# Kernel tuning notes

Hardware: AMD Instinct MI355X
Metric: run time of the kernel (lower is better)

The kernel has to match this reference:

```python
import jax, jax.numpy as jnp
import numpy as np

N_QUBITS = 6
N_SHARED_LAYERS = 3
N_TASK_LAYERS = 2
ENC_HIDDEN = 256
INPUT_DIM = 784
BATCH = 256
P1Q = 0.001  # 1-qubit depolarizing prob
P2Q = 0.01   # 2-qubit-gate depolarizing approximation (applied as 1q channel, as in source)

C = jnp.complex64
PX = jnp.array([[0, 1], [1, 0]], C)
PY = jnp.array([[0, -1j], [1j, 0]], C)
PZ = jnp.array([[1, 0], [0, -1]], C)
CNOT = jnp.array([[1, 0, 0, 0], [0, 1, 0, 0], [0, 0, 0, 1], [0, 0, 1, 0]], C)

_LOW = 'abcdefghijklmnopqrstuvwxyz'


def _apply(dm, G, axes, batched):
    # contract gate G (rows=out, cols=in) into dm along absolute dm axes `axes`
    k = len(axes)
    G = G.reshape(G.shape[:G.ndim - 2] + (2,) * (2 * k))
    nd = dm.ndim - 1  # 2 * n_qubits
    dm_sub = ['Z'] + list(_LOW[:nd])
    out_sub = list(dm_sub)
    new = 'ABCD'
    gout, gin = [], []
    for j, ax in enumerate(axes):
        gout.append(new[j]); gin.append(dm_sub[ax]); out_sub[ax] = new[j]
    g_str = ('Z' if batched else '') + ''.join(gout) + ''.join(gin)
    return jnp.einsum(f"{g_str},{''.join(dm_sub)}->{''.join(out_sub)}", G, dm)


def apply_unitary(dm, U, wires, n, batched=False):
    # rho -> U rho U^dagger; ket axes are 1+w, bra axes 1+n+w
    dm = _apply(dm, U, [1 + w for w in wires], batched)
    return _apply(dm, jnp.conj(U), [1 + n + w for w in wires], batched)


def depolarize(dm, p, q, n):
    x = apply_unitary(dm, PX, [q], n)
    y = apply_unitary(dm, PY, [q], n)
    z = apply_unitary(dm, PZ, [q], n)
    return (1.0 - p) * dm + (p / 3.0) * (x + y + z)


def rot_mat(phi, theta, omega):
    # PennyLane Rot(phi, theta, omega) = RZ(omega) RY(theta) RZ(phi)
    c = jnp.cos(theta / 2)
    s = jnp.sin(theta / 2)
    ep = jnp.exp(-0.5j * (phi + omega))  # e^{-i(phi+omega)/2}
    em = jnp.exp(0.5j * (phi - omega))   # e^{+i(phi-omega)/2}
    return jnp.stack([jnp.stack([ep * c, -em * s]),
                      jnp.stack([jnp.conj(em) * s, jnp.conj(ep) * c])]).astype(C)


def ry_batched(theta):
    # theta: (B,) -> (B,2,2)
    c = jnp.cos(theta / 2)
    s = jnp.sin(theta / 2)
    return jnp.stack([jnp.stack([c, -s], -1),
                      jnp.stack([s, c], -1)], -2).astype(C)


def strongly_entangling(dm, w, n):
    # PennyLane StronglyEntanglingLayers, default ranges r = (l % (n-1)) + 1, CNOT ring
    L = w.shape[0]
    for l in range(L):
        for i in range(n):
            dm = apply_unitary(dm, rot_mat(w[l, i, 0], w[l, i, 1], w[l, i, 2]), [i], n)
        r = (l % (n - 1)) + 1
        for i in range(n):
            dm = apply_unitary(dm, CNOT, [i, (i + r) % n], n)
    return dm


def circuit(z, shared_w, task_w):
    n = N_QUBITS
    Bz = z.shape[0]
    dm = jnp.zeros((Bz,) + (2,) * (2 * n), C).at[(slice(None),) + (0,) * (2 * n)].set(1.0)
    for i in range(n):
        dm = apply_unitary(dm, ry_batched(z[:, i] * jnp.pi), [i], n, batched=True)
        dm = depolarize(dm, P1Q, i, n)
    dm = strongly_entangling(dm, shared_w, n)
    for i in range(n):
        dm = depolarize(dm, P1Q, i, n)
    for i in range(n - 1):
        dm = depolarize(dm, P2Q, i, n)
    dm = strongly_entangling(dm, task_w, n)
    for i in range(n):
        dm = depolarize(dm, P1Q, i, n)
    D = 2 ** n
    probs = jnp.real(jnp.diagonal(dm.reshape(Bz, D, D), axis1=1, axis2=2))  # (B, D)
    bits = (jnp.arange(D)[:, None] >> jnp.arange(n - 1, -1, -1)[None, :]) & 1  # wire 0 = MSB
    signs = (1 - 2 * bits).astype(jnp.float32)  # (D, n)
    return probs.astype(jnp.float32) @ signs    # (B, n) = <Z_i>


def setup_inputs():
    key = jax.random.key(0)
    ks = jax.random.split(key, 8)
    f = jnp.float32
    return {
        "x": jax.random.normal(ks[0], (BATCH, INPUT_DIM), f),
        "W1": jax.random.normal(ks[1], (ENC_HIDDEN, INPUT_DIM), f) * 0.03,
        "b1": jnp.zeros((ENC_HIDDEN,), f),
        "ln_g": jnp.ones((ENC_HIDDEN,), f),
        "ln_b": jnp.zeros((ENC_HIDDEN,), f),
        "W2": jax.random.normal(ks[2], (N_QUBITS, ENC_HIDDEN), f) * 0.05,
        "b2": jnp.zeros((N_QUBITS,), f),
        "shared_w": jax.random.normal(ks[3], (N_SHARED_LAYERS, N_QUBITS, 3), f) * 0.1,
        "task_w": jax.random.normal(ks[4], (N_TASK_LAYERS, N_QUBITS, 3), f) * 0.1,
        "Wp": jax.random.normal(ks[5], (2, N_QUBITS), f) * 0.1,
        "bp": jnp.zeros((2,), f),
    }


def reference(x, W1, b1, ln_g, ln_b, W2, b2, shared_w, task_w, Wp, bp):
    # encoder: Linear -> ReLU -> LayerNorm -> Linear -> Tanh
    h = jnp.maximum(x @ W1.T + b1, 0.0)
    mu = h.mean(-1, keepdims=True)
    var = ((h - mu) ** 2).mean(-1, keepdims=True)
    h = (h - mu) / jnp.sqrt(var + 1e-5) * ln_g + ln_b
    z = jnp.tanh(h @ W2.T + b2)            # (B, N_QUBITS)
    ev = circuit(z, shared_w, task_w)      # (B, N_QUBITS)
    return ev @ Wp.T + bp                  # (B, 2)
```

## Files before the change

### kernel.cpp

```cpp
#include <hip/hip_runtime.h>
#include <math.h>

#define NQ 6
#define BLK 1024
#define HID 256
#define INDIM 784

#define PW1 0.001f
#define PW2 0.01f
constexpr float WO1 = 1.f - 4.f * PW1 / 3.f;
constexpr float WO2 = 1.f - 4.f * PW2 / 3.f;
constexpr float WOc = WO1 * WO2;

struct alignas(16) RingTabs { int t[3][4096]; };
constexpr RingTabs make_ring_tabs() {
    RingTabs R{};
    for (int ri = 0; ri < 3; ++ri) {
        int r = ri + 1;
        for (int v = 0; v < 4096; ++v) {
            int x[6], z[6];
            for (int w = 0; w < 6; ++w) { x[w] = (v >> (2 * w + 1)) & 1; z[w] = (v >> (2 * w)) & 1; }
            int sgn = 0;
            for (int i = 5; i >= 0; --i) {
                int c = i, tg = (i + r) % 6;
                sgn ^= x[c] & z[tg] & (x[tg] ^ z[c] ^ 1);
                x[tg] ^= x[c];
                z[c]  ^= z[tg];
            }
            int s = 0;
            for (int w = 0; w < 6; ++w) s |= (x[w] << (2 * w + 1)) | (z[w] << (2 * w));
            R.t[ri][v] = s | (sgn << 31);
        }
    }
    return R;
}
static __device__ const RingTabs RT = make_ring_tabs();

__device__ __forceinline__ int swz(int n) {
    return n ^ ((((n >> 6) ^ (n >> 10)) & 3) << 3);
}

template<int CTRL>
__device__ __forceinline__ float qb(float v) {
    int r = __builtin_amdgcn_update_dpp(0, __builtin_bit_cast(int, v), CTRL, 0xF, 0xF, true);
    return __builtin_bit_cast(float, r);
}

__device__ __forceinline__ void rot_reg(float e[4], float4 rZ, float4 rX, float4 rY) {
    float X = e[2], Y = e[3], Z = e[1];
    e[2] = fmaf(rX.x, X, fmaf(rX.y, Y, rX.z * Z));
    e[3] = fmaf(rY.x, X, fmaf(rY.y, Y, rY.z * Z));
    e[1] = fmaf(rZ.x, X, fmaf(rZ.y, Y, rZ.z * Z));
}

__device__ __forceinline__ void rot_lane(float e[4], float4 cf) {
    #pragma unroll
    for (int j = 0; j < 4; ++j) {
        float vZ = qb<0x55>(e[j]);
        float vX = qb<0xAA>(e[j]);
        float vY = qb<0xFF>(e[j]);
        e[j] = fmaf(cf.x, vX, fmaf(cf.y, vY, fmaf(cf.z, vZ, cf.w * e[j])));
    }
}


__global__ __launch_bounds__(BLK)
void nqm_kernel(const float* __restrict__ x, const float* __restrict__ W1,
                const float* __restrict__ b1, const float* __restrict__ ln_g,
                const float* __restrict__ ln_b, const float* __restrict__ W2,
                const float* __restrict__ b2, const float* __restrict__ shared_w,
                const float* __restrict__ task_w, const float* __restrict__ Wp,
                const float* __restrict__ bp, float* __restrict__ out)
{
    __shared__ __align__(16) float dm[4096];
    __shared__ float4 xrow[INDIM / 4];
    __shared__ float hpart[1024];
    __shared__ __align__(16) float4 Mlane[30][4];
    __shared__ float bloch[NQ][4];
    __shared__ float red[4], red2[4];
    __shared__ float zpart[4][8];
    __shared__ float bcast[2];
    __shared__ float evs[8];

    const int tid = threadIdx.x;
    const int b = blockIdx.x;
    const int lane = tid & 63;
    const int qpos = tid & 3;

    if (tid < INDIM / 4) xrow[tid] = ((const float4*)(x + (size_t)b * INDIM))[tid];
    __syncthreads();

    {
        const int u = tid & 255, p = tid >> 8;
        const float4* w1v = (const float4*)(W1 + (size_t)u * INDIM) + p * 49;
        const float4* xv4 = xrow + p * 49;
        float acc = 0.0f;
        #pragma unroll 7
        for (int k = 0; k < 49; ++k) {
            float4 wv = w1v[k];
            float4 xv = xv4[k];
            acc = fmaf(wv.x, xv.x, acc);
            acc = fmaf(wv.y, xv.y, acc);
            acc = fmaf(wv.z, xv.z, acc);
            acc = fmaf(wv.w, xv.w, acc);
        }
        hpart[p * 256 + u] = acc;
    }
    __syncthreads();

    float h = 0.0f;
    if (tid < 256) {
        h = hpart[tid] + hpart[256 + tid] + hpart[512 + tid] + hpart[768 + tid] + b1[tid];
        h = fmaxf(h, 0.0f);
        float s = h, s2 = h * h;
        #pragma unroll
        for (int off = 32; off > 0; off >>= 1) {
            s  += __shfl_down(s, off, 64);
            s2 += __shfl_down(s2, off, 64);
        }
        if (lane == 0) { red[tid >> 6] = s; red2[tid >> 6] = s2; }
    }
    __syncthreads();
    if (tid == 0) {
        float ts  = red[0] + red[1] + red[2] + red[3];
        float ts2 = red2[0] + red2[1] + red2[2] + red2[3];
        float mu  = ts * (1.0f / HID);
        float var = ts2 * (1.0f / HID) - mu * mu;
        bcast[0] = mu;
        bcast[1] = rsqrtf(var + 1e-5f);
    }
    __syncthreads();
    if (tid < 256) {
        float hnj = (h - bcast[0]) * bcast[1] * ln_g[tid] + ln_b[tid];
        float p[NQ];
        #pragma unroll
        for (int i = 0; i < NQ; ++i) p[i] = hnj * W2[i * HID + tid];
        #pragma unroll
        for (int off = 32; off > 0; off >>= 1) {
            #pragma unroll
            for (int i = 0; i < NQ; ++i) p[i] += __shfl_down(p[i], off, 64);
        }
        if (lane == 0) {
            #pragma unroll
            for (int i = 0; i < NQ; ++i) zpart[tid >> 6][i] = p[i];
        }
    }
    __syncthreads();

    if (tid < NQ) {
        float z = zpart[0][tid] + zpart[1][tid] + zpart[2][tid] + zpart[3][tid] + b2[tid];
        z = tanhf(z);
        float sn, c;
        sincosf(z * 3.14159265358979323846f, &sn, &c);
        bloch[tid][0] = 1.0f;
        bloch[tid][1] = WO1 * c;
        bloch[tid][2] = WO1 * sn;
        bloch[tid][3] = 0.0f;
    } else if (tid < 36) {
        int g = tid - NQ;
        int layer = g / NQ;
        int wire = g % NQ;
        const float* w = (layer < 3) ? (shared_w + (layer * NQ + wire) * 3)
                                     : (task_w + ((layer - 3) * NQ + wire) * 3);
        float phi = w[0], theta = w[1], omega = w[2];
        float sf, cf_, st, ct, so, co;
        sincosf(phi, &sf, &cf_);
        sincosf(theta, &st, &ct);
        sincosf(omega, &so, &co);
        float M00 = co * ct * cf_ - so * sf;
        float M01 = -co * ct * sf - so * cf_;
        float M02 = co * st;
        float M10 = so * ct * cf_ + co * sf;
        float M11 = -so * ct * sf + co * cf_;
        float M12 = so * st;
        float M20 = -st * cf_;
        float M21 = st * sf;
        float M22 = ct;
        float f = (layer == 3) ? ((wire < 5) ? WOc : WO1) : 1.0f;
        Mlane[g][0] = make_float4(0.f, 0.f, 0.f, 1.f);
        Mlane[g][1] = make_float4(f * M20, f * M21, f * M22, 0.f);
        Mlane[g][2] = make_float4(f * M00, f * M01, f * M02, 0.f);
        Mlane[g][3] = make_float4(f * M10, f * M11, f * M12, 0.f);
    }

    const int t = tid;
    const int base1 = ((t & 0x3C0) << 2) | ((t & 3) << 6) | ((t >> 2) & 0xF);
    const int base2 = ((t & 3) << 10) | ((t >> 2) & 0xFF);
    __syncthreads();

    const int rtab[4] = {0, 1, 2, 0};
    for (int l = 0; l < 5; ++l) {
        const int g0 = l * 6;
        float e[4];

        if (l == 0) {
            float A = bloch[1][t & 3] * bloch[2][(t >> 2) & 3] * bloch[3][(t >> 4) & 3]
                    * bloch[4][(t >> 6) & 3] * bloch[5][(t >> 8) & 3];
            e[0] = A * bloch[0][0];
            e[1] = A * bloch[0][1];
            e[2] = A * bloch[0][2];
            e[3] = A * bloch[0][3];
        } else {
            const int4 te = *(const int4*)&RT.t[rtab[l - 1]][t << 2];
            float v0 = dm[swz(te.x & 4095)];
            float v1 = dm[swz(te.y & 4095)];
            float v2 = dm[swz(te.z & 4095)];
            float v3 = dm[swz(te.w & 4095)];
            e[0] = __int_as_float(__float_as_int(v0) ^ (te.x & 0x80000000));
            e[1] = __int_as_float(__float_as_int(v1) ^ (te.y & 0x80000000));
            e[2] = __int_as_float(__float_as_int(v2) ^ (te.z & 0x80000000));
            e[3] = __int_as_float(__float_as_int(v3) ^ (te.w & 0x80000000));
            __syncthreads();
        }
        {
            float4 rZ = Mlane[g0 + 0][1], rX = Mlane[g0 + 0][2], rY = Mlane[g0 + 0][3];
            rot_reg(e, rZ, rX, rY);
            rot_lane(e, Mlane[g0 + 1][qpos]);
        }
        *(float4*)&dm[swz(t << 2)] = make_float4(e[0], e[1], e[2], e[3]);
        __syncthreads();

        e[0] = dm[swz(base1)];
        e[1] = dm[swz(base1 + 16)];
        e[2] = dm[swz(base1 + 32)];
        e[3] = dm[swz(base1 + 48)];
        {
            float4 rZ = Mlane[g0 + 2][1], rX = Mlane[g0 + 2][2], rY = Mlane[g0 + 2][3];
            rot_reg(e, rZ, rX, rY);
            rot_lane(e, Mlane[g0 + 3][qpos]);
        }
        dm[swz(base1)]      = e[0];
        dm[swz(base1 + 16)] = e[1];
        dm[swz(base1 + 32)] = e[2];
        dm[swz(base1 + 48)] = e[3];
        __syncthreads();

        e[0] = dm[swz(base2)];
        e[1] = dm[swz(base2 + 256)];
        e[2] = dm[swz(base2 + 512)];
        e[3] = dm[swz(base2 + 768)];
        {
            float4 rZ = Mlane[g0 + 4][1], rX = Mlane[g0 + 4][2], rY = Mlane[g0 + 4][3];
            rot_reg(e, rZ, rX, rY);
            rot_lane(e, Mlane[g0 + 5][qpos]);
        }
        dm[swz(base2)]       = e[0];
        dm[swz(base2 + 256)] = e[1];
        dm[swz(base2 + 512)] = e[2];
        dm[swz(base2 + 768)] = e[3];
        __syncthreads();
    }

    if (tid < NQ) {
        int e = RT.t[1][1 << (2 * tid)];
        float v = dm[swz(e & 4095)];
        v = __int_as_float(__float_as_int(v) ^ (e & 0x80000000));
        evs[tid] = WO1 * v;
    }
    __syncthreads();
    if (tid < 2) {
        float o = bp[tid];
        #pragma unroll
        for (int i = 0; i < NQ; ++i) o = fmaf(evs[i], Wp[tid * NQ + i], o);
        out[b * 2 + tid] = o;
    }
}

extern "C" void kernel_launch(void* const* d_in, const int* in_sizes, int n_in,
                              void* d_out, int out_size, void* d_ws, size_t ws_size,
                              hipStream_t stream) {
    (void)in_sizes; (void)n_in; (void)d_ws; (void)ws_size; (void)out_size;
    const float* x        = (const float*)d_in[0];
    const float* W1       = (const float*)d_in[1];
    const float* b1       = (const float*)d_in[2];
    const float* ln_g     = (const float*)d_in[3];
    const float* ln_b     = (const float*)d_in[4];
    const float* W2       = (const float*)d_in[5];
    const float* b2       = (const float*)d_in[6];
    const float* shared_w = (const float*)d_in[7];
    const float* task_w   = (const float*)d_in[8];
    const float* Wp       = (const float*)d_in[9];
    const float* bp       = (const float*)d_in[10];
    float* out = (float*)d_out;

    hipLaunchKernelGGL(nqm_kernel, dim3(256), dim3(BLK), 0, stream,
                       x, W1, b1, ln_g, ln_b, W2, b2, shared_w, task_w, Wp, bp, out);
}
```

Before: 102.5 us.

## Apply four qubit rotations in-register via cross-lane ops and double-buffer density matrix

The density-matrix layer used three LDS round-trips per layer. It now applies the rotations for qubits 0-3 in registers, using DPP quad broadcasts, ds_swizzle and shfl across lanes. The remaining two qubits go through a single transposed LDS pass. Ping-pong buffers (dmA/dmB) remove the extra barrier before writing, cutting barriers per layer from four to two, in exchange for more LDS usage and costlier cross-lane shuffles.

```diff
diff --git a/kernel.cpp b/kernel.cpp
--- a/kernel.cpp
+++ b/kernel.cpp
@@ -45,6 +45,10 @@
     int r = __builtin_amdgcn_update_dpp(0, __builtin_bit_cast(int, v), CTRL, 0xF, 0xF, true);
     return __builtin_bit_cast(float, r);
 }
+template<int OFF>
+__device__ __forceinline__ float swzl(float v) {
+    return __builtin_bit_cast(float, __builtin_amdgcn_ds_swizzle(__builtin_bit_cast(int, v), OFF));
+}
 
 __device__ __forceinline__ void rot_reg(float e[4], float4 rZ, float4 rX, float4 rY) {
     float X = e[2], Y = e[3], Z = e[1];
@@ -52,13 +56,31 @@
     e[3] = fmaf(rY.x, X, fmaf(rY.y, Y, rY.z * Z));
     e[1] = fmaf(rZ.x, X, fmaf(rZ.y, Y, rZ.z * Z));
 }
-
-__device__ __forceinline__ void rot_lane(float e[4], float4 cf) {
+__device__ __forceinline__ void rot_q1(float e[4], float4 cf) {
     #pragma unroll
     for (int j = 0; j < 4; ++j) {
         float vZ = qb<0x55>(e[j]);
         float vX = qb<0xAA>(e[j]);
         float vY = qb<0xFF>(e[j]);
+        e[j] = fmaf(cf.x, vX, fmaf(cf.y, vY, fmaf(cf.z, vZ, cf.w * e[j])));
+    }
+}
+__device__ __forceinline__ void rot_q2(float e[4], float4 cf) {
+    #pragma unroll
+    for (int j = 0; j < 4; ++j) {
+        float vZ = swzl<0x093>(e[j]);
+        float vX = swzl<0x113>(e[j]);
+        float vY = swzl<0x193>(e[j]);
+        e[j] = fmaf(cf.x, vX, fmaf(cf.y, vY, fmaf(cf.z, vZ, cf.w * e[j])));
+    }
+}
+__device__ __forceinline__ void rot_q3(float e[4], float4 cf, int lane) {
+    int s1 = (lane & 15) | 16, s2 = (lane & 15) | 32, s3 = (lane & 15) | 48;
+    #pragma unroll
+    for (int j = 0; j < 4; ++j) {
+        float vZ = __shfl(e[j], s1, 64);
+        float vX = __shfl(e[j], s2, 64);
+        float vY = __shfl(e[j], s3, 64);
         e[j] = fmaf(cf.x, vX, fmaf(cf.y, vY, fmaf(cf.z, vZ, cf.w * e[j])));
     }
 }
@@ -72,7 +94,8 @@
                 const float* __restrict__ task_w, const float* __restrict__ Wp,
                 const float* __restrict__ bp, float* __restrict__ out)
 {
-    __shared__ __align__(16) float dm[4096];
+    __shared__ __align__(16) float dmA[4096];
+    __shared__ __align__(16) float dmB[4096];
     __shared__ float4 xrow[INDIM / 4];
     __shared__ float hpart[1024];
     __shared__ __align__(16) float4 Mlane[30][4];
@@ -84,8 +107,8 @@
 
     const int tid = threadIdx.x;
     const int b = blockIdx.x;
+    const int wv = tid >> 6;
     const int lane = tid & 63;
-    const int qpos = tid & 3;
 
     if (tid < INDIM / 4) xrow[tid] = ((const float4*)(x + (size_t)b * INDIM))[tid];
     __syncthreads();
@@ -97,12 +120,12 @@
         float acc = 0.0f;
         #pragma unroll 7
         for (int k = 0; k < 49; ++k) {
-            float4 wv = w1v[k];
+            float4 wvv = w1v[k];
             float4 xv = xv4[k];
-            acc = fmaf(wv.x, xv.x, acc);
-            acc = fmaf(wv.y, xv.y, acc);
-            acc = fmaf(wv.z, xv.z, acc);
-            acc = fmaf(wv.w, xv.w, acc);
+            acc = fmaf(wvv.x, xv.x, acc);
+            acc = fmaf(wvv.y, xv.y, acc);
+            acc = fmaf(wvv.z, xv.z, acc);
+            acc = fmaf(wvv.w, xv.w, acc);
         }
         hpart[p * 256 + u] = acc;
     }
@@ -183,77 +206,56 @@
         Mlane[g][3] = make_float4(f * M10, f * M11, f * M12, 0.f);
     }
 
-    const int t = tid;
-    const int base1 = ((t & 0x3C0) << 2) | ((t & 3) << 6) | ((t >> 2) & 0xF);
-    const int base2 = ((t & 3) << 10) | ((t >> 2) & 0xFF);
-    __syncthreads();
-
+    const int q1 = lane & 3, q2 = (lane >> 2) & 3, q3 = (lane >> 4) & 3;
+    const int q4 = wv & 3, q5 = wv >> 2;
+    const int baseB = ((lane & 3) << 10) | (wv << 4) | (lane >> 2);
     const int rtab[4] = {0, 1, 2, 0};
+    __syncthreads();
+
     for (int l = 0; l < 5; ++l) {
         const int g0 = l * 6;
         float e[4];
 
         if (l == 0) {
-            float A = bloch[1][t & 3] * bloch[2][(t >> 2) & 3] * bloch[3][(t >> 4) & 3]
-                    * bloch[4][(t >> 6) & 3] * bloch[5][(t >> 8) & 3];
+            float A = bloch[1][q1] * bloch[2][q2] * bloch[3][q3] * bloch[4][q4] * bloch[5][q5];
             e[0] = A * bloch[0][0];
             e[1] = A * bloch[0][1];
             e[2] = A * bloch[0][2];
             e[3] = A * bloch[0][3];
         } else {
-            const int4 te = *(const int4*)&RT.t[rtab[l - 1]][t << 2];
-            float v0 = dm[swz(te.x & 4095)];
-            float v1 = dm[swz(te.y & 4095)];
-            float v2 = dm[swz(te.z & 4095)];
-            float v3 = dm[swz(te.w & 4095)];
+            const int4 te = *(const int4*)&RT.t[rtab[l - 1]][tid << 2];
+            float v0 = dmA[swz(te.x & 4095)];
+            float v1 = dmA[swz(te.y & 4095)];
+            float v2 = dmA[swz(te.z & 4095)];
+            float v3 = dmA[swz(te.w & 4095)];
             e[0] = __int_as_float(__float_as_int(v0) ^ (te.x & 0x80000000));
             e[1] = __int_as_float(__float_as_int(v1) ^ (te.y & 0x80000000));
             e[2] = __int_as_float(__float_as_int(v2) ^ (te.z & 0x80000000));
             e[3] = __int_as_float(__float_as_int(v3) ^ (te.w & 0x80000000));
-            __syncthreads();
-        }
-        {
-            float4 rZ = Mlane[g0 + 0][1], rX = Mlane[g0 + 0][2], rY = Mlane[g0 + 0][3];
-            rot_reg(e, rZ, rX, rY);
-            rot_lane(e, Mlane[g0 + 1][qpos]);
-        }
-        *(float4*)&dm[swz(t << 2)] = make_float4(e[0], e[1], e[2], e[3]);
+        }
+        rot_reg(e, Mlane[g0 + 0][1], Mlane[g0 + 0][2], Mlane[g0 + 0][3]);
+        rot_q1(e, Mlane[g0 + 1][q1]);
+        rot_q2(e, Mlane[g0 + 2][q2]);
+        rot_q3(e, Mlane[g0 + 3][q3], lane);
+        *(float4*)&dmB[swz(tid << 2)] = make_float4(e[0], e[1], e[2], e[3]);
         __syncthreads();
 
-        e[0] = dm[swz(base1)];
-        e[1] = dm[swz(base1 + 16)];
-        e[2] = dm[swz(base1 + 32)];
-        e[3] = dm[swz(base1 + 48)];
-        {
-            float4 rZ = Mlane[g0 + 2][1], rX = Mlane[g0 + 2][2], rY = Mlane[g0 + 2][3];
-            rot_reg(e, rZ, rX, rY);
-            rot_lane(e, Mlane[g0 + 3][qpos]);
-        }
-        dm[swz(base1)]      = e[0];
-        dm[swz(base1 + 16)] = e[1];
-        dm[swz(base1 + 32)] = e[2];
-        dm[swz(base1 + 48)] = e[3];
-        __syncthreads();
-
-        e[0] = dm[swz(base2)];
-        e[1] = dm[swz(base2 + 256)];
-        e[2] = dm[swz(base2 + 512)];
-        e[3] = dm[swz(base2 + 768)];
-        {
-            float4 rZ = Mlane[g0 + 4][1], rX = Mlane[g0 + 4][2], rY = Mlane[g0 + 4][3];
-            rot_reg(e, rZ, rX, rY);
-            rot_lane(e, Mlane[g0 + 5][qpos]);
-        }
-        dm[swz(base2)]       = e[0];
-        dm[swz(base2 + 256)] = e[1];
-        dm[swz(base2 + 512)] = e[2];
-        dm[swz(base2 + 768)] = e[3];
+        e[0] = dmB[swz(baseB)];
+        e[1] = dmB[swz(baseB + 256)];
+        e[2] = dmB[swz(baseB + 512)];
+        e[3] = dmB[swz(baseB + 768)];
+        rot_reg(e, Mlane[g0 + 4][1], Mlane[g0 + 4][2], Mlane[g0 + 4][3]);
+        rot_q1(e, Mlane[g0 + 5][lane & 3]);
+        dmA[swz(baseB)]       = e[0];
+        dmA[swz(baseB + 256)] = e[1];
+        dmA[swz(baseB + 512)] = e[2];
+        dmA[swz(baseB + 768)] = e[3];
         __syncthreads();
     }
 
     if (tid < NQ) {
         int e = RT.t[1][1 << (2 * tid)];
-        float v = dm[swz(e & 4095)];
+        float v = dmA[swz(e & 4095)];
         v = __int_as_float(__float_as_int(v) ^ (e & 0x80000000));
         evs[tid] = WO1 * v;
     }
```

Result: no change. 103.2 us (+0.7%).
